# Performance work log

Hardware: AMD Instinct MI355X
Metric: run time of the kernel (lower is better)

The kernel has to match this reference:

```python
import jax, jax.numpy as jnp
import numpy as np
import math

B, T, C = 1, 4096, 1024
N_HEAD = 16
HEAD_DIM = C // N_HEAD


def _rotate_every_two(x):
    x1 = x[..., ::2]
    x2 = x[..., 1::2]
    return jnp.stack((-x2, x1), axis=-1).reshape(x.shape)


def setup_inputs() -> dict:
    key = jax.random.key(0)
    k1, k2, k3 = jax.random.split(key, 3)
    s = 0.02
    return {
        "x": jax.random.normal(k1, (B, T, C), dtype=jnp.float32),
        "Wqkv": jax.random.normal(k2, (C, 3 * C), dtype=jnp.float32) * s,
        "bqkv": jnp.zeros((3 * C,), dtype=jnp.float32),
        "Wproj": jax.random.normal(k3, (C, C), dtype=jnp.float32) * s,
        "bproj": jnp.zeros((C,), dtype=jnp.float32),
    }


def reference(x, Wqkv, bqkv, Wproj, bproj):
    b, t, c = x.shape
    qkv = x @ Wqkv + bqkv                      # [B,T,3C]
    q, k, v = jnp.split(qkv, 3, axis=2)
    # [B,H,T,D]
    q = q.reshape(b, t, N_HEAD, HEAD_DIM).transpose(0, 2, 1, 3)
    k = k.reshape(b, t, N_HEAD, HEAD_DIM).transpose(0, 2, 1, 3)
    v = v.reshape(b, t, N_HEAD, HEAD_DIM).transpose(0, 2, 1, 3)

    # RoPE (as in source: emb = cat(freqs, freqs), rotate_every_two interleaved)
    inv_freq = 1.0 / (10000.0 ** (jnp.arange(0, HEAD_DIM, 2, dtype=jnp.float32) / HEAD_DIM))
    pos = jnp.arange(t, dtype=jnp.float32)
    freqs = pos[:, None] * inv_freq[None, :]          # [T, D/2]
    emb = jnp.concatenate((freqs, freqs), axis=-1)    # [T, D]
    cos = jnp.cos(emb)[None, None, :, :]
    sin = jnp.sin(emb)[None, None, :, :]
    q = q * cos + _rotate_every_two(q) * sin
    k = k * cos + _rotate_every_two(k) * sin

    att = jnp.einsum('bhqd,bhkd->bhqk', q, k) / math.sqrt(HEAD_DIM)
    causal = jnp.tril(jnp.ones((t, t), dtype=bool))
    att = jnp.where(causal[None, None], att, -jnp.inf)
    att = jax.nn.softmax(att, axis=-1)
    y = jnp.einsum('bhqk,bhkd->bhqd', att, v)         # [B,H,T,D]
    y = y.transpose(0, 2, 1, 3).reshape(b, t, c)
    return y @ Wproj + bproj
```

## Files before the change

kernel.cpp:

```cpp
#include <hip/hip_runtime.h>
#include <hip/hip_bf16.h>
#include <cstdint>
#include <cstddef>

constexpr int TSEQ = 4096;
constexpr int CDIM = 1024;
constexpr int NHEAD = 16;
constexpr int HDIM = 64;
constexpr float QSCALE = 0.125f * 1.4426950408889634f;

using bf16 = __hip_bfloat16;
typedef __bf16 bf16x8 __attribute__((ext_vector_type(8)));
typedef float floatx4 __attribute__((ext_vector_type(4)));

__device__ inline uint32_t cvt_pk_bf16(float a, float b) {
  uint32_t r;
  asm("v_cvt_pk_bf16_f32 %0, %1, %2" : "=v"(r) : "v"(a), "v"(b));
  return r;
}
__device__ inline floatx4 vadd4(floatx4 a, floatx4 b) {
  floatx4 r;
  r[0] = a[0] + b[0]; r[1] = a[1] + b[1];
  r[2] = a[2] + b[2]; r[3] = a[3] + b[3];
  return r;
}
__device__ inline void gload_lds16(const bf16* g, bf16* l) {
  __builtin_amdgcn_global_load_lds(
      (const __attribute__((address_space(1))) void*)g,
      (__attribute__((address_space(3))) void*)l, 16, 0, 0);
}
__device__ inline void atomic_pk_add_bf16(bf16* addr, uint32_t data) {
  asm volatile("global_atomic_pk_add_bf16 %0, %1, off"
               :: "v"(addr), "v"(data) : "memory");
}

__global__ __launch_bounds__(256) void f32_to_bf16(
    const float4* __restrict__ in, uint64_t* __restrict__ out, int n4) {
  const int i = blockIdx.x * 256 + threadIdx.x;
  if (i < n4) {
    const float4 v = in[i];
    union { bf16 h[4]; uint64_t u; } p;
    p.h[0] = __float2bfloat16(v.x);
    p.h[1] = __float2bfloat16(v.y);
    p.h[2] = __float2bfloat16(v.z);
    p.h[3] = __float2bfloat16(v.w);
    out[i] = p.u;
  }
}

__global__ __launch_bounds__(256) void rope_table(float* __restrict__ tab) {
  const int i = blockIdx.x * 256 + threadIdx.x;
  const int t = i >> 5, j = i & 31;
  const float invf = exp2f((float)j * (-2.0f / 64.0f) * 13.287712379549449f);
  float sn, cs;
  sincosf((float)t * invf, &sn, &cs);
  tab[t * 64 + j] = cs;
  tab[t * 64 + 32 + j] = sn;
}

__global__ __launch_bounds__(256) void transpose_f32_bf16(
    const float* __restrict__ in, bf16* __restrict__ out, int R, int C) {
  __shared__ float tile[32][33];
  const int c0 = blockIdx.x * 32, r0 = blockIdx.y * 32;
  const int tx = threadIdx.x, ty = threadIdx.y;
#pragma unroll
  for (int i = 0; i < 32; i += 8)
    tile[ty + i][tx] = in[(size_t)(r0 + ty + i) * C + c0 + tx];
  __syncthreads();
#pragma unroll
  for (int i = 0; i < 32; i += 8)
    out[(size_t)(c0 + ty + i) * R + r0 + tx] = __float2bfloat16(tile[tx][ty + i]);
}

template <int MODE>
__global__ __launch_bounds__(256) void gemm_bt(
    const bf16* __restrict__ A, const bf16* __restrict__ Bt,
    const float* __restrict__ bias, const float* __restrict__ tab,
    float* __restrict__ Cout,
    bf16* __restrict__ Qh, bf16* __restrict__ Kh, bf16* __restrict__ Vt,
    int M, int N, int K) {
  __shared__ __align__(16) bf16 smem[4 * 64 * 72];
  bf16* As = smem;
  bf16* Bs = smem + 128 * 64;
  const int tid = threadIdx.x;
  const int m0 = blockIdx.y * 128, n0 = blockIdx.x * 128;
  const int wave = tid >> 6, lane = tid & 63;
  const int l15 = lane & 15, quad = lane >> 4;
  const int wm = (wave >> 1) * 64, wn = (wave & 1) * 64;

  const floatx4 fzero = {0.f, 0.f, 0.f, 0.f};
  floatx4 acc[4][4];
#pragma unroll
  for (int mi = 0; mi < 4; mi++)
#pragma unroll
    for (int ni = 0; ni < 4; ni++) acc[mi][ni] = fzero;

  const int gr = lane >> 3;
  const int gcs = ((lane & 7) ^ gr) << 3;
  const bf16* Ag = A + (size_t)(m0 + wave * 32 + gr) * K + gcs;
  const bf16* Bg = Bt + (size_t)(n0 + wave * 32 + gr) * K + gcs;
  bf16* Asw = As + wave * 32 * 64;
  bf16* Bsw = Bs + wave * 32 * 64;

  const int x7f = l15 & 7;
  const int af0 = (quad ^ x7f) << 3;
  const int af1 = ((4 + quad) ^ x7f) << 3;

  for (int k0 = 0; k0 < K; k0 += 64) {
    __syncthreads();
#pragma unroll
    for (int j = 0; j < 4; j++) {
      gload_lds16(Ag + (size_t)j * 8 * K + k0, Asw + j * 512);
      gload_lds16(Bg + (size_t)j * 8 * K + k0, Bsw + j * 512);
    }
    __syncthreads();

    bf16x8 a[4][2], b[4][2];
#pragma unroll
    for (int mi = 0; mi < 4; mi++) {
      const bf16* ar = As + (wm + mi * 16 + l15) * 64;
      a[mi][0] = *(const bf16x8*)(ar + af0);
      a[mi][1] = *(const bf16x8*)(ar + af1);
    }
#pragma unroll
    for (int ni = 0; ni < 4; ni++) {
      const bf16* br = Bs + (wn + ni * 16 + l15) * 64;
      b[ni][0] = *(const bf16x8*)(br + af0);
      b[ni][1] = *(const bf16x8*)(br + af1);
    }
#pragma unroll
    for (int kk = 0; kk < 2; kk++)
#pragma unroll
      for (int mi = 0; mi < 4; mi++)
#pragma unroll
        for (int ni = 0; ni < 4; ni++)
          acc[mi][ni] = __builtin_amdgcn_mfma_f32_16x16x32_bf16(
              a[mi][kk], b[ni][kk], acc[mi][ni], 0, 0, 0);
  }

  __syncthreads();

  if (MODE == 1) {
    bf16* ep = smem + (size_t)wave * (64 * 72);
    const int cbase = n0 + wn;
    const int sec = cbase >> 10;
    const int hh = (cbase & 1023) >> 6;
    if (sec == 2) {
#pragma unroll
      for (int ni = 0; ni < 4; ni++) {
        const int d = ni * 16 + l15;
        const float bv = bias[cbase + d];
#pragma unroll
        for (int mi = 0; mi < 4; mi++) {
          const uint32_t lo =
              cvt_pk_bf16(acc[mi][ni][0] + bv, acc[mi][ni][1] + bv);
          const uint32_t hi =
              cvt_pk_bf16(acc[mi][ni][2] + bv, acc[mi][ni][3] + bv);
          *(uint64_t*)(ep + (size_t)d * 72 + mi * 16 + quad * 4) =
              (uint64_t)lo | ((uint64_t)hi << 32);
        }
      }
      __asm__ __volatile__("" ::: "memory");
#pragma unroll
      for (int it = 0; it < 8; it++) {
        const int dr = it * 8 + (lane >> 3);
        const int t8 = (lane & 7) * 8;
        const bf16x8 vv = *(const bf16x8*)(ep + (size_t)dr * 72 + t8);
        *(bf16x8*)(Vt + ((size_t)hh * HDIM + dr) * TSEQ + m0 + wm + t8) = vv;
      }
    } else {
      bf16* dst = (sec == 0) ? Qh : Kh;
      const float postscale = (sec == 0) ? QSCALE : 1.0f;
#pragma unroll
      for (int ni = 0; ni < 4; ni++) {
        const int c = ni * 16 + l15;
        const float bv = bias[cbase + c];
        const int j = c & 31;
#pragma unroll
        for (int mi = 0; mi < 4; mi++) {
#pragma unroll
          for (int r = 0; r < 4; r++) {
            const int t = m0 + wm + mi * 16 + quad * 4 + r;
            const float v = acc[mi][ni][r] + bv;
            const float partner = __shfl_xor(v, 1, 64);
            const float cs = tab[t * 64 + j];
            const float sn = tab[t * 64 + 32 + j];
            const float res =
                (v * cs + ((c & 1) ? partner : -partner) * sn) * postscale;
            ep[(size_t)(mi * 16 + quad * 4 + r) * 72 + c] =
                __float2bfloat16(res);
          }
        }
      }
      __asm__ __volatile__("" ::: "memory");
#pragma unroll
      for (int it = 0; it < 8; it++) {
        const int row = it * 8 + (lane >> 3);
        const int c8 = (lane & 7) * 8;
        const bf16x8 vv = *(const bf16x8*)(ep + (size_t)row * 72 + c8);
        *(bf16x8*)(dst + ((size_t)hh * TSEQ + m0 + wm + row) * HDIM + c8) = vv;
      }
    }
  } else {
    float* ep32 = (float*)smem + (size_t)wave * (32 * 68);
    float bvv[4];
#pragma unroll
    for (int ni = 0; ni < 4; ni++) bvv[ni] = bias[n0 + wn + ni * 16 + l15];
#pragma unroll
    for (int half = 0; half < 2; half++) {
      if (half) __asm__ __volatile__("" ::: "memory");
#pragma unroll
      for (int ni = 0; ni < 4; ni++)
#pragma unroll
        for (int mi2 = 0; mi2 < 2; mi2++)
#pragma unroll
          for (int r = 0; r < 4; r++)
            ep32[(size_t)(mi2 * 16 + quad * 4 + r) * 68 + ni * 16 + l15] =
                acc[half * 2 + mi2][ni][r] + bvv[ni];
      __asm__ __volatile__("" ::: "memory");
#pragma unroll
      for (int it = 0; it < 8; it++) {
        const int row = it * 4 + (lane >> 4);
        const float4 vv = *(const float4*)(ep32 + (size_t)row * 68 + l15 * 4);
        *(float4*)(Cout + (size_t)(m0 + wm + half * 32 + row) * N + n0 + wn +
                   l15 * 4) = vv;
      }
    }
  }
}

__global__ __launch_bounds__(256) void attn_kernel(
    const bf16* __restrict__ Qh, const bf16* __restrict__ Kh,
    const bf16* __restrict__ Vt, bf16* __restrict__ Yacc,
    float* __restrict__ Lacc) {
  const int h = blockIdx.y;
  const int s = blockIdx.x;
  const int p = s >> 1, half = s & 1;
  const int tile_lo = p, tile_hi = 63 - p;
  const int tid = threadIdx.x;
  const int w = tid >> 6, lane = tid & 63;
  const int l15 = lane & 15, quad = lane >> 4;
  const int q_lo = tile_lo * 64 + w * 16 + l15;
  const int q_hi = tile_hi * 64 + w * 16 + l15;
  const int nkv_lo = tile_lo + 1;
  const int nkv_hi = tile_hi + 1;
  const int mid = (nkv_lo >= 17) ? 17 : (33 - nkv_lo);
  const int beg = half ? mid : 0;
  const int end = half ? nkv_hi : mid;
  const bool any_lo = beg < nkv_lo;

  const bf16* Qb = Qh + (size_t)h * TSEQ * HDIM;
  const bf16* Kb = Kh + (size_t)h * TSEQ * HDIM;
  const bf16* Vb = Vt + (size_t)h * HDIM * TSEQ;

  __shared__ __align__(16) bf16 Ks[2][64 * 64];
  __shared__ __align__(16) bf16 Vs[2][64 * 64];
  __shared__ bf16 Plds[4][32][72];

  const int sr = tid >> 3;
  const int sc = tid & 7;
  const int sp = sc << 3;
  const int sofs = sr * 64 + ((sc ^ (sr & 7)) << 3);

  bf16x8 Rk0, Rk1, Rv0, Rv1;
  auto stage_load = [&](int kv0) {
    Rk0 = *(const bf16x8*)(Kb + (size_t)(kv0 + sr) * HDIM + sp);
    Rk1 = *(const bf16x8*)(Kb + (size_t)(kv0 + sr + 32) * HDIM + sp);
    Rv0 = *(const bf16x8*)(Vb + (size_t)sr * TSEQ + kv0 + sp);
    Rv1 = *(const bf16x8*)(Vb + (size_t)(sr + 32) * TSEQ + kv0 + sp);
  };
  auto stage_write = [&](int buf) {
    *(bf16x8*)(Ks[buf] + sofs) = Rk0;
    *(bf16x8*)(Ks[buf] + sofs + 32 * 64) = Rk1;
    *(bf16x8*)(Vs[buf] + sofs) = Rv0;
    *(bf16x8*)(Vs[buf] + sofs + 32 * 64) = Rv1;
  };

  const int x7 = l15 & 7;
  const int fofs0 = ((quad ^ x7) << 3);
  const int fofs1 = (((4 + quad) ^ x7) << 3);

  bf16x8 qf[2][2];
#pragma unroll
  for (int ks = 0; ks < 2; ks++) {
    qf[0][ks] = *(const bf16x8*)(Qb + (size_t)q_lo * HDIM + ks * 32 + quad * 8);
    qf[1][ks] = *(const bf16x8*)(Qb + (size_t)q_hi * HDIM + ks * 32 + quad * 8);
  }

  const floatx4 fzero = {0.f, 0.f, 0.f, 0.f};
  floatx4 o[2][4];
  floatx4 lacc[2] = {fzero, fzero};
#pragma unroll
  for (int qt = 0; qt < 2; qt++)
#pragma unroll
    for (int dt = 0; dt < 4; dt++) o[qt][dt] = fzero;

  auto exp_tile = [&](floatx4* s2, int qrow, bool maskit, int kv0, int qt) {
    if (maskit) {
#pragma unroll
      for (int kt = 0; kt < 4; kt++)
#pragma unroll
        for (int r = 0; r < 4; r++) {
          const int kv = kv0 + kt * 16 + quad * 4 + r;
          if (kv > qrow) s2[kt][r] = -1e30f;
        }
    }
#pragma unroll
    for (int kt = 0; kt < 4; kt++)
#pragma unroll
      for (int r = 0; r < 4; r++)
        s2[kt][r] = __builtin_amdgcn_exp2f(s2[kt][r]);
    lacc[qt] = vadd4(lacc[qt], vadd4(vadd4(s2[0], s2[1]), vadd4(s2[2], s2[3])));
#pragma unroll
    for (int kt = 0; kt < 4; kt++) {
      const uint32_t lo = cvt_pk_bf16(s2[kt][0], s2[kt][1]);
      const uint32_t hi = cvt_pk_bf16(s2[kt][2], s2[kt][3]);
      *(uint64_t*)(&Plds[w][qt * 16 + l15][kt * 16 + quad * 4]) =
          (uint64_t)lo | ((uint64_t)hi << 32);
    }
  };

  stage_load(beg * 64);
  stage_write(0);
  __syncthreads();

  int cur = 0;
  for (int kb = beg; kb < end; kb++) {
    const int kv0 = kb * 64;
    const bool lo_on = (kb < nkv_lo);
    const bool have_next = (kb + 1 < end);

    if (have_next) stage_load(kv0 + 64);

    floatx4 sh[4], sl[4];
#pragma unroll
    for (int kt = 0; kt < 4; kt++) { sh[kt] = fzero; sl[kt] = fzero; }
    __builtin_amdgcn_s_setprio(1);
#pragma unroll
    for (int kt = 0; kt < 4; kt++) {
      const bf16* krow = Ks[cur] + (kt * 16 + l15) * 64;
      const bf16x8 kf0 = *(const bf16x8*)(krow + fofs0);
      const bf16x8 kf1 = *(const bf16x8*)(krow + fofs1);
      sh[kt] = __builtin_amdgcn_mfma_f32_16x16x32_bf16(
          kf0, qf[1][0], sh[kt], 0, 0, 0);
      sh[kt] = __builtin_amdgcn_mfma_f32_16x16x32_bf16(
          kf1, qf[1][1], sh[kt], 0, 0, 0);
      if (lo_on) {
        sl[kt] = __builtin_amdgcn_mfma_f32_16x16x32_bf16(
            kf0, qf[0][0], sl[kt], 0, 0, 0);
        sl[kt] = __builtin_amdgcn_mfma_f32_16x16x32_bf16(
            kf1, qf[0][1], sl[kt], 0, 0, 0);
      }
    }
    __builtin_amdgcn_s_setprio(0);

    exp_tile(sh, q_hi, kb == nkv_hi - 1, kv0, 1);
    if (lo_on) exp_tile(sl, q_lo, kb == nkv_lo - 1, kv0, 0);
    __asm__ __volatile__("" ::: "memory");

    bf16x8 ph[2], pl[2];
#pragma unroll
    for (int ks = 0; ks < 2; ks++)
      ph[ks] = *(const bf16x8*)(&Plds[w][16 + l15][ks * 32 + quad * 8]);
    if (lo_on) {
#pragma unroll
      for (int ks = 0; ks < 2; ks++)
        pl[ks] = *(const bf16x8*)(&Plds[w][l15][ks * 32 + quad * 8]);
    }
    __builtin_amdgcn_s_setprio(1);
#pragma unroll
    for (int dt = 0; dt < 4; dt++) {
      const bf16* vrow = Vs[cur] + (dt * 16 + l15) * 64;
      const bf16x8 vf0 = *(const bf16x8*)(vrow + fofs0);
      const bf16x8 vf1 = *(const bf16x8*)(vrow + fofs1);
      o[1][dt] = __builtin_amdgcn_mfma_f32_16x16x32_bf16(
          vf0, ph[0], o[1][dt], 0, 0, 0);
      o[1][dt] = __builtin_amdgcn_mfma_f32_16x16x32_bf16(
          vf1, ph[1], o[1][dt], 0, 0, 0);
      if (lo_on) {
        o[0][dt] = __builtin_amdgcn_mfma_f32_16x16x32_bf16(
            vf0, pl[0], o[0][dt], 0, 0, 0);
        o[0][dt] = __builtin_amdgcn_mfma_f32_16x16x32_bf16(
            vf1, pl[1], o[0][dt], 0, 0, 0);
      }
    }
    __builtin_amdgcn_s_setprio(0);

    if (have_next) stage_write(cur ^ 1);
    __syncthreads();
    cur ^= 1;
  }

#pragma unroll
  for (int qt = 0; qt < 2; qt++) {
    if (qt == 0 && !any_lo) continue;
    const int q = (qt == 0) ? q_lo : q_hi;
    float l = (lacc[qt][0] + lacc[qt][1]) + (lacc[qt][2] + lacc[qt][3]);
    l += __shfl_xor(l, 16, 64);
    l += __shfl_xor(l, 32, 64);
    if (quad == 0) atomicAdd(&Lacc[(size_t)h * TSEQ + q], l);
#pragma unroll
    for (int dt = 0; dt < 4; dt++) {
      const uint32_t lo = cvt_pk_bf16(o[qt][dt][0], o[qt][dt][1]);
      const uint32_t hi = cvt_pk_bf16(o[qt][dt][2], o[qt][dt][3]);
      bf16* dst = Yacc + (size_t)q * CDIM + h * HDIM + dt * 16 + quad * 4;
      atomic_pk_add_bf16(dst, lo);
      atomic_pk_add_bf16(dst + 2, hi);
    }
  }
}

__global__ __launch_bounds__(256) void attn_norm(
    bf16* __restrict__ Y, const float* __restrict__ L) {
  const int i = blockIdx.x * 256 + threadIdx.x;
  const int q = i >> 7;
  const int c8 = (i & 127) << 3;
  const float inv = 1.0f / L[(size_t)(c8 >> 6) * TSEQ + q];
  union { bf16x8 v; bf16 e[8]; uint32_t u[4]; } x;
  x.v = *(const bf16x8*)(Y + (size_t)q * CDIM + c8);
#pragma unroll
  for (int j = 0; j < 4; j++) {
    const float a = __bfloat162float(x.e[2 * j]) * inv;
    const float b = __bfloat162float(x.e[2 * j + 1]) * inv;
    x.u[j] = cvt_pk_bf16(a, b);
  }
  *(bf16x8*)(Y + (size_t)q * CDIM + c8) = x.v;
}

extern "C" void kernel_launch(void* const* d_in, const int* in_sizes, int n_in,
                              void* d_out, int out_size, void* d_ws,
                              size_t ws_size, hipStream_t stream) {
  const float* x     = (const float*)d_in[0];
  const float* Wqkv  = (const float*)d_in[1];
  const float* bqkv  = (const float*)d_in[2];
  const float* Wproj = (const float*)d_in[3];
  const float* bproj = (const float*)d_in[4];
  float* out = (float*)d_out;

  char* ws = (char*)d_ws;
  bf16* xb     = (bf16*)(ws);
  bf16* Y      = (bf16*)(ws);
  bf16* WqkvT  = (bf16*)(ws + (8ull  << 20));
  float* Lacc  = (float*)(ws + (8ull << 20));
  bf16* WprojT = (bf16*)(ws + (14ull << 20));
  float* tab   = (float*)(ws + (14ull << 20));
  bf16* Qh     = (bf16*)(ws + (16ull << 20));
  bf16* Kh     = (bf16*)(ws + (24ull << 20));
  bf16* Vt     = (bf16*)(ws + (32ull << 20));

  f32_to_bf16<<<dim3(4096), 256, 0, stream>>>((const float4*)x, (uint64_t*)xb,
                                              TSEQ * CDIM / 4);
  transpose_f32_bf16<<<dim3(96, 32), dim3(32, 8), 0, stream>>>(
      Wqkv, WqkvT, CDIM, 3 * CDIM);
  rope_table<<<dim3(TSEQ * 32 / 256), 256, 0, stream>>>(tab);
  gemm_bt<1><<<dim3(24, 32), 256, 0, stream>>>(
      xb, WqkvT, bqkv, tab, (float*)nullptr, Qh, Kh, Vt, TSEQ, 3 * CDIM, CDIM);
  transpose_f32_bf16<<<dim3(32, 32), dim3(32, 8), 0, stream>>>(
      Wproj, WprojT, CDIM, CDIM);
  hipMemsetAsync(Y, 0, (size_t)TSEQ * CDIM * sizeof(bf16), stream);
  hipMemsetAsync(Lacc, 0, (size_t)NHEAD * TSEQ * sizeof(float), stream);
  attn_kernel<<<dim3(64, 16), 256, 0, stream>>>(Qh, Kh, Vt, Y, Lacc);
  attn_norm<<<dim3(TSEQ * CDIM / 8 / 256), 256, 0, stream>>>(Y, Lacc);
  gemm_bt<0><<<dim3(8, 32), 256, 0, stream>>>(
      Y, WprojT, bproj, (float*)nullptr, out, (bf16*)nullptr, (bf16*)nullptr,
      (bf16*)nullptr, TSEQ, CDIM, CDIM);
}
```

Before: 274.4 us.

## Single-buffer K/V shared tiles and XOR-swizzle the P staging buffer

Replaces the double-buffered K/V shared-memory tiles with single buffers. A barrier is added before each register-to-LDS write, which roughly halves LDS use and may let more blocks share a CU. The P scratch buffer drops its padded 72-column rows for a 64-column layout with an XOR swizzle that matches the fragment read offsets, aiming to avoid bank conflicts without padding. The cost is an extra __syncthreads per KV tile and less overlap between LDS writes and compute.

```diff
diff --git a/kernel.cpp b/kernel.cpp
--- a/kernel.cpp
+++ b/kernel.cpp
@@ -253,9 +253,9 @@
   const bf16* Kb = Kh + (size_t)h * TSEQ * HDIM;
   const bf16* Vb = Vt + (size_t)h * HDIM * TSEQ;
 
-  __shared__ __align__(16) bf16 Ks[2][64 * 64];
-  __shared__ __align__(16) bf16 Vs[2][64 * 64];
-  __shared__ bf16 Plds[4][32][72];
+  __shared__ __align__(16) bf16 Ks[64 * 64];
+  __shared__ __align__(16) bf16 Vs[64 * 64];
+  __shared__ __align__(16) bf16 Plds[4][32 * 64];
 
   const int sr = tid >> 3;
   const int sc = tid & 7;
@@ -269,11 +269,11 @@
     Rv0 = *(const bf16x8*)(Vb + (size_t)sr * TSEQ + kv0 + sp);
     Rv1 = *(const bf16x8*)(Vb + (size_t)(sr + 32) * TSEQ + kv0 + sp);
   };
-  auto stage_write = [&](int buf) {
-    *(bf16x8*)(Ks[buf] + sofs) = Rk0;
-    *(bf16x8*)(Ks[buf] + sofs + 32 * 64) = Rk1;
-    *(bf16x8*)(Vs[buf] + sofs) = Rv0;
-    *(bf16x8*)(Vs[buf] + sofs + 32 * 64) = Rv1;
+  auto stage_write = [&]() {
+    *(bf16x8*)(Ks + sofs) = Rk0;
+    *(bf16x8*)(Ks + sofs + 32 * 64) = Rk1;
+    *(bf16x8*)(Vs + sofs) = Rv0;
+    *(bf16x8*)(Vs + sofs + 32 * 64) = Rv1;
   };
 
   const int x7 = l15 & 7;
@@ -294,6 +294,9 @@
   for (int qt = 0; qt < 2; qt++)
 #pragma unroll
     for (int dt = 0; dt < 4; dt++) o[qt][dt] = fzero;
+
+  bf16* pw = Plds[w];
+  const int pw_off = ((quad & 1) << 2);
 
   auto exp_tile = [&](floatx4* s2, int qrow, bool maskit, int kv0, int qt) {
     if (maskit) {
@@ -311,20 +314,21 @@
       for (int r = 0; r < 4; r++)
         s2[kt][r] = __builtin_amdgcn_exp2f(s2[kt][r]);
     lacc[qt] = vadd4(lacc[qt], vadd4(vadd4(s2[0], s2[1]), vadd4(s2[2], s2[3])));
+    const int prow = qt * 16 + l15;
 #pragma unroll
     for (int kt = 0; kt < 4; kt++) {
       const uint32_t lo = cvt_pk_bf16(s2[kt][0], s2[kt][1]);
       const uint32_t hi = cvt_pk_bf16(s2[kt][2], s2[kt][3]);
-      *(uint64_t*)(&Plds[w][qt * 16 + l15][kt * 16 + quad * 4]) =
+      const int c16 = (kt * 2 + (quad >> 1)) ^ x7;
+      *(uint64_t*)(pw + prow * 64 + (c16 << 3) + pw_off) =
           (uint64_t)lo | ((uint64_t)hi << 32);
     }
   };
 
   stage_load(beg * 64);
-  stage_write(0);
+  stage_write();
   __syncthreads();
 
-  int cur = 0;
   for (int kb = beg; kb < end; kb++) {
     const int kv0 = kb * 64;
     const bool lo_on = (kb < nkv_lo);
@@ -338,7 +342,7 @@
     __builtin_amdgcn_s_setprio(1);
 #pragma unroll
     for (int kt = 0; kt < 4; kt++) {
-      const bf16* krow = Ks[cur] + (kt * 16 + l15) * 64;
+      const bf16* krow = Ks + (kt * 16 + l15) * 64;
       const bf16x8 kf0 = *(const bf16x8*)(krow + fofs0);
       const bf16x8 kf1 = *(const bf16x8*)(krow + fofs1);
       sh[kt] = __builtin_amdgcn_mfma_f32_16x16x32_bf16(
@@ -359,18 +363,16 @@
     __asm__ __volatile__("" ::: "memory");
 
     bf16x8 ph[2], pl[2];
-#pragma unroll
-    for (int ks = 0; ks < 2; ks++)
-      ph[ks] = *(const bf16x8*)(&Plds[w][16 + l15][ks * 32 + quad * 8]);
+    ph[0] = *(const bf16x8*)(pw + (16 + l15) * 64 + fofs0);
+    ph[1] = *(const bf16x8*)(pw + (16 + l15) * 64 + fofs1);
     if (lo_on) {
-#pragma unroll
-      for (int ks = 0; ks < 2; ks++)
-        pl[ks] = *(const bf16x8*)(&Plds[w][l15][ks * 32 + quad * 8]);
+      pl[0] = *(const bf16x8*)(pw + l15 * 64 + fofs0);
+      pl[1] = *(const bf16x8*)(pw + l15 * 64 + fofs1);
     }
     __builtin_amdgcn_s_setprio(1);
 #pragma unroll
     for (int dt = 0; dt < 4; dt++) {
-      const bf16* vrow = Vs[cur] + (dt * 16 + l15) * 64;
+      const bf16* vrow = Vs + (dt * 16 + l15) * 64;
       const bf16x8 vf0 = *(const bf16x8*)(vrow + fofs0);
       const bf16x8 vf1 = *(const bf16x8*)(vrow + fofs1);
       o[1][dt] = __builtin_amdgcn_mfma_f32_16x16x32_bf16(
@@ -386,9 +388,11 @@
     }
     __builtin_amdgcn_s_setprio(0);
 
-    if (have_next) stage_write(cur ^ 1);
-    __syncthreads();
-    cur ^= 1;
+    if (have_next) {
+      __syncthreads();
+      stage_write();
+      __syncthreads();
+    }
   }
 
 #pragma unroll
```

Measured after the change: 274.7 us. Within noise of the previous version (+0.1%).
